# Performance work log

Measured on AMD Instinct MI355X. Metric: run time of the kernel, lower is better.

The kernel has to match this reference:

```python
import jax, jax.numpy as jnp
import numpy as np

B, S, D = 4, 2048, 1024
H = 16
HD = D // H  # 64
SCALE = HD ** 0.5
LN_EPS = 1e-5


def setup_inputs() -> dict:
    key = jax.random.key(0)
    ks = jax.random.split(key, 13)
    std = 1.0 / np.sqrt(D)
    inp = {
        'q': jax.random.normal(ks[0], (B, S, D), jnp.float32),
        'k': jax.random.normal(ks[1], (B, S, D), jnp.float32),
        'v': jax.random.normal(ks[2], (B, S, D), jnp.float32),
        'Wq': jax.random.normal(ks[3], (D, D), jnp.float32) * std,
        'bq': jnp.zeros((D,), jnp.float32),
        'Wk': jax.random.normal(ks[4], (D, D), jnp.float32) * std,
        'bk': jnp.zeros((D,), jnp.float32),
        'Wv': jax.random.normal(ks[5], (D, D), jnp.float32) * std,
        'bv': jnp.zeros((D,), jnp.float32),
        'Wp': jax.random.normal(ks[6], (D, D), jnp.float32) * std,
        'bp': jnp.zeros((D,), jnp.float32),
        'gamma': jnp.ones((D,), jnp.float32),
        'beta': jnp.zeros((D,), jnp.float32),
    }
    return inp


def reference(q, k, v, Wq, bq, Wk, bk, Wv, bv, Wp, bp, gamma, beta):
    res = q
    # QKV projections, split into heads: [B, S, H, HD]
    qh = (q @ Wq + bq).reshape(B, S, H, HD)
    kh = (k @ Wk + bk).reshape(B, S, H, HD)
    vh = (v @ Wv + bv).reshape(B, S, H, HD)
    # Full attention scores [B, H, Sq, Sk]
    scores = jnp.einsum('bqhd,bkhd->bhqk', qh, kh) / SCALE
    # Multiplicative causal mask (zeros, NOT -inf) applied post-scale
    tril = jnp.tril(jnp.ones((S, S), scores.dtype))
    scores = scores * tril
    attn = jax.nn.softmax(scores, axis=-1)
    ctx = jnp.einsum('bhqk,bkhd->bqhd', attn, vh).reshape(B, S, D)
    out = ctx @ Wp + bp + res
    # LayerNorm over last dim
    mu = out.mean(-1, keepdims=True)
    var = out.var(-1, keepdims=True)
    return (out - mu) / jnp.sqrt(var + LN_EPS) * gamma + beta
```

## Files before the change

### kernel.cpp

```cpp
#include <hip/hip_runtime.h>

#define B_  4
#define S_  2048
#define D_  1024
#define H_  16
#define HD_ 64

#define ATT_EM 3.35462627903e-4f
#define ATT_C1 0.18033688011f
#define ATT_C0 -11.5415603281f

using v8bf = __attribute__((ext_vector_type(8))) __bf16;
using v8us = __attribute__((ext_vector_type(8))) unsigned short;
using v4f  = __attribute__((ext_vector_type(4))) float;

__device__ inline float bf2f(unsigned short u) {
    union { unsigned int i; float f; } x; x.i = ((unsigned int)u) << 16; return x.f;
}
__device__ inline unsigned short f2bf(float f) {
    union { float f; unsigned int i; } x; x.f = f;
    unsigned int r = x.i + 0x7fffu + ((x.i >> 16) & 1u);
    return (unsigned short)(r >> 16);
}
__device__ inline bool gam_is_f32(const unsigned* g) { return *g == 0x3F800000u; }

__device__ inline float fexp2(float x) {
    float r; asm("v_exp_f32 %0, %1" : "=v"(r) : "v"(x)); return r;
}

__device__ inline void gload_lds16(const void* g, void* l) {
    __builtin_amdgcn_global_load_lds(
        (const __attribute__((address_space(1))) unsigned int*)g,
        (__attribute__((address_space(3))) unsigned int*)l, 16, 0, 0);
}

__global__ __launch_bounds__(1024) void transpose_w4(const void* __restrict__ W0,
                                                     const void* __restrict__ W1,
                                                     const void* __restrict__ W2,
                                                     const void* __restrict__ W3,
                                                     unsigned short* __restrict__ Wt,
                                                     const unsigned* __restrict__ gflag) {
    const bool f32 = gam_is_f32(gflag);
    const void* W = (blockIdx.z == 0) ? W0 : (blockIdx.z == 1) ? W1
                   : (blockIdx.z == 2) ? W2 : W3;
    unsigned short* out = Wt + (size_t)blockIdx.z * (D_ * D_);
    __shared__ float tile[32][33];
    const int x = threadIdx.x, y = threadIdx.y;
    const int n0 = blockIdx.x * 32, k0 = blockIdx.y * 32;
    const size_t si = (size_t)(k0 + y) * D_ + n0 + x;
    tile[y][x] = f32 ? ((const float*)W)[si] : bf2f(((const unsigned short*)W)[si]);
    __syncthreads();
    out[(size_t)(n0 + y) * D_ + k0 + x] = f2bf(tile[x][y]);
}

__global__ __launch_bounds__(256) void cvt3_k(const void* __restrict__ q,
                                              const void* __restrict__ k,
                                              const void* __restrict__ v,
                                              unsigned short* __restrict__ oq,
                                              unsigned short* __restrict__ ok,
                                              unsigned short* __restrict__ ov,
                                              const unsigned* __restrict__ gflag) {
    const bool f32 = gam_is_f32(gflag);
    const void* in = (blockIdx.y == 0) ? q : (blockIdx.y == 1) ? k : v;
    unsigned short* out = (blockIdx.y == 0) ? oq : (blockIdx.y == 1) ? ok : ov;
    const size_t i0 = ((size_t)blockIdx.x * 256 + threadIdx.x) * 16;
    if (f32) {
        const float* p = (const float*)in + i0;
        float4 fa = *(const float4*)(p);
        float4 fb = *(const float4*)(p + 4);
        float4 fc = *(const float4*)(p + 8);
        float4 fd = *(const float4*)(p + 12);
        v8us o0, o1;
        o0[0] = f2bf(fa.x); o0[1] = f2bf(fa.y); o0[2] = f2bf(fa.z); o0[3] = f2bf(fa.w);
        o0[4] = f2bf(fb.x); o0[5] = f2bf(fb.y); o0[6] = f2bf(fb.z); o0[7] = f2bf(fb.w);
        o1[0] = f2bf(fc.x); o1[1] = f2bf(fc.y); o1[2] = f2bf(fc.z); o1[3] = f2bf(fc.w);
        o1[4] = f2bf(fd.x); o1[5] = f2bf(fd.y); o1[6] = f2bf(fd.z); o1[7] = f2bf(fd.w);
        *(v8us*)(out + i0)     = o0;
        *(v8us*)(out + i0 + 8) = o1;
    } else {
        const unsigned short* p = (const unsigned short*)in + i0;
        *(v8us*)(out + i0)     = *(const v8us*)p;
        *(v8us*)(out + i0 + 8) = *(const v8us*)(p + 8);
    }
}

__global__ __launch_bounds__(256) void transpose_v_k(const unsigned short* __restrict__ Vh,
                                                     unsigned short* __restrict__ Vt) {
    const int st = blockIdx.x, bh = blockIdx.y;
    __shared__ unsigned short tile[64][72];
    const int t = threadIdx.x;
    const int r = t >> 2, c0 = (t & 3) * 16;
    const unsigned short* src = Vh + ((size_t)bh * S_ + st * 64 + r) * HD_ + c0;
    *(v8us*)&tile[r][c0]     = *(const v8us*)src;
    *(v8us*)&tile[r][c0 + 8] = *(const v8us*)(src + 8);
    __syncthreads();
    unsigned short* dst = Vt + ((size_t)bh * HD_ + r) * S_ + st * 64 + c0;
    v8us o0, o1;
#pragma unroll
    for (int j = 0; j < 8; j++) { o0[j] = tile[c0 + j][r]; o1[j] = tile[c0 + 8 + j][r]; }
    *(v8us*)dst       = o0;
    *(v8us*)(dst + 8) = o1;
}

__global__ __launch_bounds__(256) void gemmqkv_k(const unsigned short* __restrict__ Aq,
                                                 const unsigned short* __restrict__ Ak,
                                                 const unsigned short* __restrict__ Av,
                                                 const unsigned short* __restrict__ Wt,
                                                 const void* __restrict__ bq,
                                                 const void* __restrict__ bk,
                                                 const void* __restrict__ bv,
                                                 unsigned short* __restrict__ oq,
                                                 unsigned short* __restrict__ ok,
                                                 unsigned short* __restrict__ ov,
                                                 const unsigned* __restrict__ gflag) {
    const bool xf32 = gam_is_f32(gflag);

    __shared__ unsigned short As[128 * 32];
    __shared__ unsigned short Bs[128 * 32];
    const int t = threadIdx.x;
    const int lane = t & 63, wave = t >> 6;
    const int wr = (wave >> 1) * 64, wc = (wave & 1) * 64;
    const int l15 = lane & 15, quad = lane >> 4;

    const int id = (int)blockIdx.x;
    const int sw = (id & 7) * 192 + (id >> 3);
    const int ten = sw >> 9;
    const int tid = sw & 511;
    const int n0 = (tid & 7) * 128, m0 = (tid >> 3) * 128;

    const unsigned short* A = (ten == 0) ? Aq : (ten == 1) ? Ak : Av;
    const unsigned short* W = Wt + (size_t)ten * (D_ * D_);
    const void* bias        = (ten == 0) ? bq : (ten == 1) ? bk : bv;
    unsigned short* outH    = (ten == 0) ? oq : (ten == 1) ? ok : ov;

    v4f acc[4][4];
#pragma unroll
    for (int i = 0; i < 4; i++)
#pragma unroll
        for (int j = 0; j < 4; j++) { v4f z = {0.f, 0.f, 0.f, 0.f}; acc[i][j] = z; }

    const unsigned short* srcA = A + (size_t)(m0 + wave * 32 + (lane >> 2)) * D_ + (lane & 3) * 8;
    const unsigned short* srcB = W + (size_t)(n0 + wave * 32 + (lane >> 2)) * D_ + (lane & 3) * 8;
    unsigned short* dstA = As + wave * 1024;
    unsigned short* dstB = Bs + wave * 1024;

    for (int kt = 0; kt < D_; kt += 32) {
        gload_lds16(srcA + kt,            dstA);
        gload_lds16(srcA + kt + 16 * D_,  dstA + 512);
        gload_lds16(srcB + kt,            dstB);
        gload_lds16(srcB + kt + 16 * D_,  dstB + 512);
        __syncthreads();

        v8bf af[4], wf[4];
#pragma unroll
        for (int i = 0; i < 4; i++) af[i] = *(const v8bf*)&As[(wr + i * 16 + l15) * 32 + quad * 8];
#pragma unroll
        for (int j = 0; j < 4; j++) wf[j] = *(const v8bf*)&Bs[(wc + j * 16 + l15) * 32 + quad * 8];
#pragma unroll
        for (int i = 0; i < 4; i++)
#pragma unroll
            for (int j = 0; j < 4; j++)
                acc[i][j] = __builtin_amdgcn_mfma_f32_16x16x32_bf16(af[i], wf[j], acc[i][j], 0, 0, 0);
        __syncthreads();
    }

#pragma unroll
    for (int i = 0; i < 4; i++) {
#pragma unroll
        for (int j = 0; j < 4; j++) {
            const int col = n0 + wc + j * 16 + l15;
            const float bv2 = xf32 ? ((const float*)bias)[col]
                                   : bf2f(((const unsigned short*)bias)[col]);
#pragma unroll
            for (int r = 0; r < 4; r++) {
                const int row = m0 + wr + i * 16 + quad * 4 + r;
                const float v = acc[i][j][r] + bv2;
                const int b = row >> 11, s = row & (S_ - 1);
                const int h = col >> 6,  d = col & 63;
                outH[(((size_t)(b * H_ + h)) * S_ + s) * HD_ + d] = f2bf(v);
            }
        }
    }
}

__global__ __launch_bounds__(256) void gemm_k(const unsigned short* __restrict__ A,
                                              const unsigned short* __restrict__ Wt,
                                              const void* __restrict__ bias,
                                              const void* __restrict__ res,
                                              float* __restrict__ outF,
                                              const unsigned* __restrict__ gflag) {
    const bool xf32 = gam_is_f32(gflag);

    __shared__ unsigned short As[128 * 32];
    __shared__ unsigned short Bs[128 * 32];
    const int t = threadIdx.x;
    const int lane = t & 63, wave = t >> 6;
    const int wr = (wave >> 1) * 64, wc = (wave & 1) * 64;
    const int l15 = lane & 15, quad = lane >> 4;

    const int id = (int)blockIdx.x;
    const int sw = (id & 7) * 64 + (id >> 3);
    const int n0 = (sw & 7) * 128, m0 = (sw >> 3) * 128;

    v4f acc[4][4];
#pragma unroll
    for (int i = 0; i < 4; i++)
#pragma unroll
        for (int j = 0; j < 4; j++) { v4f z = {0.f, 0.f, 0.f, 0.f}; acc[i][j] = z; }

    const unsigned short* srcA = A  + (size_t)(m0 + wave * 32 + (lane >> 2)) * D_ + (lane & 3) * 8;
    const unsigned short* srcB = Wt + (size_t)(n0 + wave * 32 + (lane >> 2)) * D_ + (lane & 3) * 8;
    unsigned short* dstA = As + wave * 1024;
    unsigned short* dstB = Bs + wave * 1024;

    for (int kt = 0; kt < D_; kt += 32) {
        gload_lds16(srcA + kt,            dstA);
        gload_lds16(srcA + kt + 16 * D_,  dstA + 512);
        gload_lds16(srcB + kt,            dstB);
        gload_lds16(srcB + kt + 16 * D_,  dstB + 512);
        __syncthreads();

        v8bf af[4], wf[4];
#pragma unroll
        for (int i = 0; i < 4; i++) af[i] = *(const v8bf*)&As[(wr + i * 16 + l15) * 32 + quad * 8];
#pragma unroll
        for (int j = 0; j < 4; j++) wf[j] = *(const v8bf*)&Bs[(wc + j * 16 + l15) * 32 + quad * 8];
#pragma unroll
        for (int i = 0; i < 4; i++)
#pragma unroll
            for (int j = 0; j < 4; j++)
                acc[i][j] = __builtin_amdgcn_mfma_f32_16x16x32_bf16(af[i], wf[j], acc[i][j], 0, 0, 0);
        __syncthreads();
    }

#pragma unroll
    for (int i = 0; i < 4; i++) {
#pragma unroll
        for (int j = 0; j < 4; j++) {
            const int col = n0 + wc + j * 16 + l15;
            const float bv = xf32 ? ((const float*)bias)[col]
                                  : bf2f(((const unsigned short*)bias)[col]);
#pragma unroll
            for (int r = 0; r < 4; r++) {
                const int row = m0 + wr + i * 16 + quad * 4 + r;
                const size_t idx = (size_t)row * D_ + col;
                float v = acc[i][j][r] + bv;
                v += xf32 ? ((const float*)res)[idx]
                          : bf2f(((const unsigned short*)res)[idx]);
                outF[idx] = v;
            }
        }
    }
}

__global__ __launch_bounds__(256) void suffixv_k(const unsigned short* __restrict__ Vh,
                                                 float* __restrict__ SV) {
    const int bh = blockIdx.x;
    const int lane = threadIdx.x & 63, wave = threadIdx.x >> 6;
    __shared__ float part[32][64];
#pragma unroll
    for (int tt = 0; tt < 8; tt++) {
        const int t0 = wave * 8 + tt;
        float s = 0.f;
        const unsigned short* vp = Vh + ((size_t)bh * S_ + t0 * 64) * HD_ + lane;
#pragma unroll 8
        for (int r = 0; r < 64; r++) s += bf2f(vp[r * HD_]);
        part[t0][lane] = s;
    }
    __syncthreads();
    if (wave == 0) {
        float acc = 0.f;
        SV[((size_t)bh * 33 + 32) * 64 + lane] = 0.f;
        for (int tt = 31; tt >= 0; tt--) {
            acc += part[tt][lane];
            SV[((size_t)bh * 33 + tt) * 64 + lane] = acc;
        }
    }
}

__global__ __launch_bounds__(256) void attn_k(const unsigned short* __restrict__ Qh,
                                              const unsigned short* __restrict__ Kh,
                                              const unsigned short* __restrict__ Vt,
                                              const float* __restrict__ SV,
                                              unsigned short* __restrict__ ctx) {
    const int xa = blockIdx.x;
    const int qtA = xa, qtB = 31 - xa;
    const int bh = blockIdx.y;
    __shared__ unsigned short Ks[64][72];
    __shared__ unsigned short Vts[64][72];
    __shared__ __align__(16) unsigned short Ps[4][16][72];
    const int t = threadIdx.x, lane = t & 63, wave = t >> 6;
    const int l15 = lane & 15, quad = lane >> 4;

    const size_t headoff = (size_t)bh * S_ * HD_;

    v8bf aqA[2], aqB[2];
    {
        const unsigned short* qp = Qh + headoff + (size_t)(qtA * 64 + wave * 16 + l15) * HD_ + quad * 8;
        aqA[0] = *(const v8bf*)qp;
        aqA[1] = *(const v8bf*)(qp + 32);
        qp = Qh + headoff + (size_t)(qtB * 64 + wave * 16 + l15) * HD_ + quad * 8;
        aqB[0] = *(const v8bf*)qp;
        aqB[1] = *(const v8bf*)(qp + 32);
    }

    float lpA = 0.f, lpB = 0.f;
    v4f oA[4], oB[4];
#pragma unroll
    for (int dt = 0; dt < 4; dt++) { v4f z = {0.f, 0.f, 0.f, 0.f}; oA[dt] = z; oB[dt] = z; }

    const int srow = t >> 2, sc = (t & 3) * 16;

    v8bf kf[4][2];

    auto step = [&](const v8bf* aq, float& lp, v4f* oacc, bool diag) {
        v4f st[4];
        __builtin_amdgcn_s_setprio(1);
#pragma unroll
        for (int ct = 0; ct < 4; ct++) {
            v4f z = {0.f, 0.f, 0.f, 0.f};
#pragma unroll
            for (int kk = 0; kk < 2; kk++)
                z = __builtin_amdgcn_mfma_f32_16x16x32_bf16(kf[ct][kk], aq[kk], z, 0, 0, 0);
            st[ct] = z;
        }
        __builtin_amdgcn_s_setprio(0);

#pragma unroll
        for (int ct = 0; ct < 4; ct++) {
            float e0, e1, e2, e3;
            {
                float x0 = fexp2(fmaf(st[ct][0], ATT_C1, ATT_C0));
                float x1 = fexp2(fmaf(st[ct][1], ATT_C1, ATT_C0));
                float x2 = fexp2(fmaf(st[ct][2], ATT_C1, ATT_C0));
                float x3 = fexp2(fmaf(st[ct][3], ATT_C1, ATT_C0));
                if (diag) {
                    const int kg = ct * 16 + quad * 4;
                    const int qg = wave * 16 + l15;
                    x0 = (kg + 0 <= qg) ? x0 : ATT_EM;
                    x1 = (kg + 1 <= qg) ? x1 : ATT_EM;
                    x2 = (kg + 2 <= qg) ? x2 : ATT_EM;
                    x3 = (kg + 3 <= qg) ? x3 : ATT_EM;
                }
                e0 = x0; e1 = x1; e2 = x2; e3 = x3;
            }
            lp += (e0 + e1) + (e2 + e3);
            unsigned plo, phi;
            asm("v_cvt_pk_bf16_f32 %0, %1, %2" : "=v"(plo) : "v"(e0), "v"(e1));
            asm("v_cvt_pk_bf16_f32 %0, %1, %2" : "=v"(phi) : "v"(e2), "v"(e3));
            uint2 pw; pw.x = plo; pw.y = phi;
            *(uint2*)&Ps[wave][l15][ct * 16 + quad * 4] = pw;
        }

        asm volatile("s_waitcnt lgkmcnt(0)" ::: "memory");
        __builtin_amdgcn_sched_barrier(0);

        __builtin_amdgcn_s_setprio(1);
#pragma unroll
        for (int kk = 0; kk < 2; kk++) {
            v8bf ap = *(const v8bf*)&Ps[wave][l15][kk * 32 + quad * 8];
#pragma unroll
            for (int dt = 0; dt < 4; dt++) {
                v8bf vb = *(const v8bf*)&Vts[dt * 16 + l15][kk * 32 + quad * 8];
                oacc[dt] = __builtin_amdgcn_mfma_f32_16x16x32_bf16(ap, vb, oacc[dt], 0, 0, 0);
            }
        }
        __builtin_amdgcn_s_setprio(0);
        asm volatile("" ::: "memory");
    };

    for (int kt = 0; kt <= qtB; kt++) {
        const unsigned short* kp = Kh + headoff + (size_t)(kt * 64 + srow) * HD_ + sc;
        v8us k0 = *(const v8us*)kp, k1 = *(const v8us*)(kp + 8);
        *(v8us*)&Ks[srow][sc]     = k0;
        *(v8us*)&Ks[srow][sc + 8] = k1;
        const unsigned short* vp = Vt + headoff + (size_t)srow * S_ + kt * 64 + sc;
        v8us v0 = *(const v8us*)vp, v1 = *(const v8us*)(vp + 8);
        *(v8us*)&Vts[srow][sc]     = v0;
        *(v8us*)&Vts[srow][sc + 8] = v1;
        __syncthreads();

#pragma unroll
        for (int ct = 0; ct < 4; ct++)
#pragma unroll
            for (int kk = 0; kk < 2; kk++)
                kf[ct][kk] = *(const v8bf*)&Ks[ct * 16 + l15][kk * 32 + quad * 8];

        step(aqB, lpB, oB, kt == qtB);
        if (kt <= qtA) step(aqA, lpA, oA, kt == qtA);

        __syncthreads();
    }

    auto finish = [&](float lp, v4f* oacc, int qt) {
        lp += __shfl_xor(lp, 16);
        lp += __shfl_xor(lp, 32);
        float l_[4];
#pragma unroll
        for (int r = 0; r < 4; r++) l_[r] = __shfl(lp, quad * 4 + r);
        const int cnt = (31 - qt) * 64;
        if (cnt > 0) {
            const float* svp = SV + ((size_t)bh * 33 + (qt + 1)) * 64;
            float sv[4];
#pragma unroll
            for (int dt = 0; dt < 4; dt++) sv[dt] = svp[dt * 16 + l15];
#pragma unroll
            for (int r = 0; r < 4; r++) {
                l_[r] += (float)cnt * ATT_EM;
#pragma unroll
                for (int dt = 0; dt < 4; dt++) oacc[dt][r] += ATT_EM * sv[dt];
            }
        }
        const int bb = bh >> 4, hh = bh & 15;
#pragma unroll
        for (int dt = 0; dt < 4; dt++)
#pragma unroll
            for (int r = 0; r < 4; r++) {
                const int qrow = qt * 64 + wave * 16 + quad * 4 + r;
                const size_t idx = ((size_t)bb * S_ + qrow) * D_ + hh * HD_ + dt * 16 + l15;
                ctx[idx] = f2bf(oacc[dt][r] / l_[r]);
            }
    };
    finish(lpB, oB, qtB);
    finish(lpA, oA, qtA);
}

__global__ __launch_bounds__(256) void ln_k(const float* __restrict__ X,
                                            const void* __restrict__ gamma,
                                            const void* __restrict__ beta,
                                            void* __restrict__ outv,
                                            const unsigned* __restrict__ gflag) {
    const bool f32 = gam_is_f32(gflag);
    const int row = blockIdx.x, t = threadIdx.x;
    const float* xp = X + (size_t)row * D_;
    float4 x = *(const float4*)(xp + t * 4);
    float s = x.x + x.y + x.z + x.w;
    float q = x.x * x.x + x.y * x.y + x.z * x.z + x.w * x.w;
#pragma unroll
    for (int off = 1; off < 64; off <<= 1) {
        s += __shfl_xor(s, off);
        q += __shfl_xor(q, off);
    }
    __shared__ float red[2][4];
    const int wave = t >> 6, lane = t & 63;
    if (lane == 0) { red[0][wave] = s; red[1][wave] = q; }
    __syncthreads();
    s = red[0][0] + red[0][1] + red[0][2] + red[0][3];
    q = red[1][0] + red[1][1] + red[1][2] + red[1][3];
    const float mu = s * (1.f / 1024.f);
    const float var = q * (1.f / 1024.f) - mu * mu;
    const float rstd = rsqrtf(var + 1e-5f);
    const float* xe = &x.x;
#pragma unroll
    for (int e = 0; e < 4; e++) {
        const int c = t * 4 + e;
        const float g = f32 ? ((const float*)gamma)[c] : bf2f(((const unsigned short*)gamma)[c]);
        const float b = f32 ? ((const float*)beta)[c]  : bf2f(((const unsigned short*)beta)[c]);
        const float y = (xe[e] - mu) * rstd * g + b;
        if (f32) ((float*)outv)[(size_t)row * D_ + c] = y;
        else     ((unsigned short*)outv)[(size_t)row * D_ + c] = f2bf(y);
    }
}

extern "C" void kernel_launch(void* const* d_in, const int* in_sizes, int n_in,
                              void* d_out, int out_size, void* d_ws, size_t ws_size,
                              hipStream_t stream) {
    const void* q     = d_in[0];
    const void* k     = d_in[1];
    const void* v     = d_in[2];
    const void* Wq    = d_in[3];
    const void* bq    = d_in[4];
    const void* Wk    = d_in[5];
    const void* bk    = d_in[6];
    const void* Wv    = d_in[7];
    const void* bv    = d_in[8];
    const void* Wp    = d_in[9];
    const void* bp    = d_in[10];
    const void* gamma = d_in[11];
    const void* beta  = d_in[12];
    const unsigned* gflag = (const unsigned*)gamma;

    char* ws = (char*)d_ws;
    size_t off = 0;
    unsigned short* Wt   = (unsigned short*)(ws + off); off += (size_t)4 * 1024 * 1024 * 2;
    unsigned short* qh   = (unsigned short*)(ws + off); off += (size_t)8192 * 1024 * 2;
    unsigned short* kh   = (unsigned short*)(ws + off); off += (size_t)8192 * 1024 * 2;
    unsigned short* vh   = (unsigned short*)(ws + off); off += (size_t)8192 * 1024 * 2;
    float*          SV   = (float*)(ws + off);          off += (size_t)64 * 33 * 64 * 4;
    unsigned short* ctx  = (unsigned short*)(ws + off); off += (size_t)8192 * 1024 * 2;
    unsigned short* cvtK = (unsigned short*)(ws + off); off += (size_t)8192 * 1024 * 2;
    float* pre = (float*)qh;
    unsigned short* cvtQ = ctx;
    unsigned short* cvtV = (unsigned short*)d_out;
    unsigned short* vt = (unsigned short*)d_out;

    transpose_w4<<<dim3(32, 32, 4), dim3(32, 32), 0, stream>>>(Wq, Wk, Wv, Wp, Wt, gflag);
    cvt3_k<<<dim3(2048, 3), 256, 0, stream>>>(q, k, v, cvtQ, cvtK, cvtV, gflag);

    gemmqkv_k<<<1536, 256, 0, stream>>>(cvtQ, cvtK, cvtV, Wt, bq, bk, bv,
                                        qh, kh, vh, gflag);

    transpose_v_k<<<dim3(32, 64), 256, 0, stream>>>(vh, vt);
    suffixv_k<<<64, 256, 0, stream>>>(vh, SV);
    attn_k<<<dim3(16, 64), 256, 0, stream>>>(qh, kh, vt, SV, ctx);

    gemm_k<<<512, 256, 0, stream>>>(ctx, Wt + 3145728, bp, q, pre, gflag);

    ln_k<<<8192, 256, 0, stream>>>(pre, gamma, beta, d_out, gflag);
}
```

Baseline: 417.6 us.

## Double-buffer LDS tiles in projection GEMMs to overlap loads with MFMA

Both the QKV projection GEMM and the output projection GEMM now use two LDS buffers per operand. The next K-tile is prefetched with global_load_lds while the current one is consumed, using explicit vmcnt waits and raw barriers in place of full __syncthreads. This is meant to hide global memory latency behind the MFMA work. It doubles LDS use per block, which could lower occupancy, and the K loop is fully unrolled, which adds code size.

```diff
diff --git a/kernel.cpp b/kernel.cpp
--- a/kernel.cpp
+++ b/kernel.cpp
@@ -32,6 +32,14 @@
     __builtin_amdgcn_global_load_lds(
         (const __attribute__((address_space(1))) unsigned int*)g,
         (__attribute__((address_space(3))) unsigned int*)l, 16, 0, 0);
+}
+
+__device__ inline void waitv4() { asm volatile("s_waitcnt vmcnt(4)" ::: "memory"); }
+__device__ inline void waitv0() { asm volatile("s_waitcnt vmcnt(0)" ::: "memory"); }
+__device__ inline void barx() {
+    asm volatile("" ::: "memory");
+    __builtin_amdgcn_s_barrier();
+    asm volatile("" ::: "memory");
 }
 
 __global__ __launch_bounds__(1024) void transpose_w4(const void* __restrict__ W0,
@@ -115,8 +123,8 @@
                                                  const unsigned* __restrict__ gflag) {
     const bool xf32 = gam_is_f32(gflag);
 
-    __shared__ unsigned short As[128 * 32];
-    __shared__ unsigned short Bs[128 * 32];
+    __shared__ unsigned short As0[128 * 32], As1[128 * 32];
+    __shared__ unsigned short Bs0[128 * 32], Bs1[128 * 32];
     const int t = threadIdx.x;
     const int lane = t & 63, wave = t >> 6;
     const int wr = (wave >> 1) * 64, wc = (wave & 1) * 64;
@@ -141,27 +149,44 @@
 
     const unsigned short* srcA = A + (size_t)(m0 + wave * 32 + (lane >> 2)) * D_ + (lane & 3) * 8;
     const unsigned short* srcB = W + (size_t)(n0 + wave * 32 + (lane >> 2)) * D_ + (lane & 3) * 8;
-    unsigned short* dstA = As + wave * 1024;
-    unsigned short* dstB = Bs + wave * 1024;
-
-    for (int kt = 0; kt < D_; kt += 32) {
-        gload_lds16(srcA + kt,            dstA);
-        gload_lds16(srcA + kt + 16 * D_,  dstA + 512);
-        gload_lds16(srcB + kt,            dstB);
-        gload_lds16(srcB + kt + 16 * D_,  dstB + 512);
-        __syncthreads();
-
+    unsigned short* dA0 = As0 + wave * 1024;
+    unsigned short* dA1 = As1 + wave * 1024;
+    unsigned short* dB0 = Bs0 + wave * 1024;
+    unsigned short* dB1 = Bs1 + wave * 1024;
+
+    auto stage = [&](unsigned short* dA, unsigned short* dB, int kt) {
+        gload_lds16(srcA + kt,            dA);
+        gload_lds16(srcA + kt + 16 * D_,  dA + 512);
+        gload_lds16(srcB + kt,            dB);
+        gload_lds16(srcB + kt + 16 * D_,  dB + 512);
+    };
+    auto compute = [&](const unsigned short* AS, const unsigned short* BS) {
         v8bf af[4], wf[4];
 #pragma unroll
-        for (int i = 0; i < 4; i++) af[i] = *(const v8bf*)&As[(wr + i * 16 + l15) * 32 + quad * 8];
-#pragma unroll
-        for (int j = 0; j < 4; j++) wf[j] = *(const v8bf*)&Bs[(wc + j * 16 + l15) * 32 + quad * 8];
+        for (int i = 0; i < 4; i++) af[i] = *(const v8bf*)&AS[(wr + i * 16 + l15) * 32 + quad * 8];
+#pragma unroll
+        for (int j = 0; j < 4; j++) wf[j] = *(const v8bf*)&BS[(wc + j * 16 + l15) * 32 + quad * 8];
 #pragma unroll
         for (int i = 0; i < 4; i++)
 #pragma unroll
             for (int j = 0; j < 4; j++)
                 acc[i][j] = __builtin_amdgcn_mfma_f32_16x16x32_bf16(af[i], wf[j], acc[i][j], 0, 0, 0);
-        __syncthreads();
+    };
+
+    stage(dA0, dB0, 0);
+#pragma unroll
+    for (int k2 = 0; k2 < 16; ++k2) {
+        const int kt = k2 * 64;
+        stage(dA1, dB1, kt + 32);
+        waitv4();
+        barx();
+        compute(As0, Bs0);
+        barx();
+        if (k2 < 15) { stage(dA0, dB0, kt + 64); waitv4(); }
+        else         { waitv0(); }
+        barx();
+        compute(As1, Bs1);
+        barx();
     }
 
 #pragma unroll
@@ -191,8 +216,8 @@
                                               const unsigned* __restrict__ gflag) {
     const bool xf32 = gam_is_f32(gflag);
 
-    __shared__ unsigned short As[128 * 32];
-    __shared__ unsigned short Bs[128 * 32];
+    __shared__ unsigned short As0[128 * 32], As1[128 * 32];
+    __shared__ unsigned short Bs0[128 * 32], Bs1[128 * 32];
     const int t = threadIdx.x;
     const int lane = t & 63, wave = t >> 6;
     const int wr = (wave >> 1) * 64, wc = (wave & 1) * 64;
@@ -210,27 +235,44 @@
 
     const unsigned short* srcA = A  + (size_t)(m0 + wave * 32 + (lane >> 2)) * D_ + (lane & 3) * 8;
     const unsigned short* srcB = Wt + (size_t)(n0 + wave * 32 + (lane >> 2)) * D_ + (lane & 3) * 8;
-    unsigned short* dstA = As + wave * 1024;
-    unsigned short* dstB = Bs + wave * 1024;
-
-    for (int kt = 0; kt < D_; kt += 32) {
-        gload_lds16(srcA + kt,            dstA);
-        gload_lds16(srcA + kt + 16 * D_,  dstA + 512);
-        gload_lds16(srcB + kt,            dstB);
-        gload_lds16(srcB + kt + 16 * D_,  dstB + 512);
-        __syncthreads();
-
+    unsigned short* dA0 = As0 + wave * 1024;
+    unsigned short* dA1 = As1 + wave * 1024;
+    unsigned short* dB0 = Bs0 + wave * 1024;
+    unsigned short* dB1 = Bs1 + wave * 1024;
+
+    auto stage = [&](unsigned short* dA, unsigned short* dB, int kt) {
+        gload_lds16(srcA + kt,            dA);
+        gload_lds16(srcA + kt + 16 * D_,  dA + 512);
+        gload_lds16(srcB + kt,            dB);
+        gload_lds16(srcB + kt + 16 * D_,  dB + 512);
+    };
+    auto compute = [&](const unsigned short* AS, const unsigned short* BS) {
         v8bf af[4], wf[4];
 #pragma unroll
-        for (int i = 0; i < 4; i++) af[i] = *(const v8bf*)&As[(wr + i * 16 + l15) * 32 + quad * 8];
-#pragma unroll
-        for (int j = 0; j < 4; j++) wf[j] = *(const v8bf*)&Bs[(wc + j * 16 + l15) * 32 + quad * 8];
+        for (int i = 0; i < 4; i++) af[i] = *(const v8bf*)&AS[(wr + i * 16 + l15) * 32 + quad * 8];
+#pragma unroll
+        for (int j = 0; j < 4; j++) wf[j] = *(const v8bf*)&BS[(wc + j * 16 + l15) * 32 + quad * 8];
 #pragma unroll
         for (int i = 0; i < 4; i++)
 #pragma unroll
             for (int j = 0; j < 4; j++)
                 acc[i][j] = __builtin_amdgcn_mfma_f32_16x16x32_bf16(af[i], wf[j], acc[i][j], 0, 0, 0);
-        __syncthreads();
+    };
+
+    stage(dA0, dB0, 0);
+#pragma unroll
+    for (int k2 = 0; k2 < 16; ++k2) {
+        const int kt = k2 * 64;
+        stage(dA1, dB1, kt + 32);
+        waitv4();
+        barx();
+        compute(As0, Bs0);
+        barx();
+        if (k2 < 15) { stage(dA0, dB0, kt + 64); waitv4(); }
+        else         { waitv0(); }
+        barx();
+        compute(As1, Bs1);
+        barx();
     }
 
 #pragma unroll
```

Result: no change. 417.5 us (-0.0%).
